# Kernel tuning notes

Hardware: AMD Instinct MI355X
Metric: run time of the kernel (lower is better)

The kernel has to match this reference:

```python
import jax, jax.numpy as jnp
import numpy as np

B, T, E, STRIDE = 32, 4096, 256, 16


def setup_inputs() -> dict:
    key = jax.random.key(0)
    nn_outs = jax.random.normal(key, (B, T, E), dtype=jnp.float32)
    # cut marker (==1) every STRIDE tokens, last position of each segment
    batch_x = jnp.zeros((B, T), dtype=jnp.int64).at[:, STRIDE - 1::STRIDE].set(1)
    return {"nn_outs": nn_outs, "batch_x": batch_x}


def reference(nn_outs, batch_x):
    """Hierarchical pooling: mean-pool nn_outs over segments delimited by
    batch_x == 1. Segment k of a row spans (cut_{k-1}, cut_k] inclusive of the
    cut token; tokens after the last cut are dropped (as in the original).
    Returns (pooled (B, maxlen, E), n_segments (B,))."""
    b, t, e = nn_outs.shape
    is_cut = (batch_x == 1)
    n_cuts = jnp.sum(is_cut, axis=1)                      # (B,) segments per row
    # exclusive cumsum: segment id of token t = #cuts strictly before t
    seg = jnp.cumsum(is_cut, axis=1) - is_cut.astype(jnp.int64)  # (B, T)
    valid = seg < n_cuts[:, None]                         # tokens after last cut dropped
    maxlen = int(jnp.max(n_cuts))                         # padded interm_step
    # flatten to global segment ids; invalid tokens go to a dump bucket
    gseg = jnp.where(valid, seg + jnp.arange(b, dtype=jnp.int64)[:, None] * maxlen,
                     b * maxlen)
    gseg = gseg.reshape(-1)
    flat = nn_outs.reshape(b * t, e)
    n_seg_total = b * maxlen + 1
    sums = jax.ops.segment_sum(flat, gseg, num_segments=n_seg_total)[:-1]
    counts = jax.ops.segment_sum(valid.reshape(-1).astype(nn_outs.dtype), gseg,
                                 num_segments=n_seg_total)[:-1]
    pooled = sums / jnp.maximum(counts, 1)[:, None]       # empty pad segments -> 0
    return pooled.reshape(b, maxlen, e), n_cuts
```

## Files before the change

### kernel.cpp

```cpp
#include <hip/hip_runtime.h>

#define NROWS 32
#define TLEN  4096
#define EDIM  256
#define PER   (TLEN / 256)
#define SEGS_PER_BLOCK 4

__global__ __launch_bounds__(256) void fused_pool_kernel(
    const float* __restrict__ nn,
    const int*  __restrict__ batch_x,
    int maxlen, int nb_per_row,
    float* __restrict__ out,
    float* __restrict__ n_cuts_out)
{
    const int tid  = threadIdx.x;
    const int lane = tid & 63;
    const int w    = tid >> 6;
    const int blk  = blockIdx.x;
    const int b    = blk / nb_per_row;
    const int k0   = (blk - b * nb_per_row) * SEGS_PER_BLOCK;

    __shared__ int s_cuts[TLEN];
    __shared__ int s_wsum[4];

    const int* row = batch_x + (long long)b * TLEN;
    const int t0 = tid * PER;

    int flags[PER];
#pragma unroll
    for (int j = 0; j < PER; j += 4) {
        const int4 v = *(const int4*)(row + t0 + j);
        flags[j] = v.x; flags[j + 1] = v.y; flags[j + 2] = v.z; flags[j + 3] = v.w;
    }
    int local = 0;
#pragma unroll
    for (int j = 0; j < PER; ++j) local += (flags[j] == 1);

    int incl = local;
#pragma unroll
    for (int d = 1; d < 64; d <<= 1) {
        const int v = __shfl_up(incl, d, 64);
        if (lane >= d) incl += v;
    }
    if (lane == 63) s_wsum[w] = incl;
    __syncthreads();
    const int s0 = s_wsum[0], s1 = s_wsum[1], s2 = s_wsum[2], s3 = s_wsum[3];
    const int wbase = (w > 0 ? s0 : 0) + (w > 1 ? s1 : 0) + (w > 2 ? s2 : 0);
    const int ncuts = s0 + s1 + s2 + s3;

    int idx = wbase + incl - local;
#pragma unroll
    for (int j = 0; j < PER; ++j)
        if (flags[j] == 1) s_cuts[idx++] = t0 + j;
    __syncthreads();

    if (k0 == 0 && tid == 0) n_cuts_out[b] = (float)ncuts;

    const int k = k0 + w;
    if (k >= maxlen) return;

    float4 acc = make_float4(0.f, 0.f, 0.f, 0.f);
    if (k < ncuts) {
        const int start = (k == 0) ? 0 : (s_cuts[k - 1] + 1);
        const int end   = s_cuts[k];
        const int cnt   = end - start + 1;
        const float* base = nn + ((long long)b * TLEN + start) * EDIM + lane * 4;

        if (cnt == 16) {
            float4 v[16];
#pragma unroll
            for (int t = 0; t < 16; ++t)
                v[t] = *(const float4*)(base + (long long)t * EDIM);
#pragma unroll
            for (int s = 1; s < 16; s <<= 1)
#pragma unroll
                for (int t = 0; t < 16; t += 2 * s) {
                    v[t].x += v[t + s].x; v[t].y += v[t + s].y;
                    v[t].z += v[t + s].z; v[t].w += v[t + s].w;
                }
            const float inv = 1.0f / 16.0f;
            acc.x = v[0].x * inv; acc.y = v[0].y * inv;
            acc.z = v[0].z * inv; acc.w = v[0].w * inv;
        } else {
            float4 a0 = make_float4(0.f, 0.f, 0.f, 0.f);
            float4 a1 = a0, a2 = a0, a3 = a0;
            int t = 0;
            for (; t + 4 <= cnt; t += 4) {
                const float4 v0 = *(const float4*)(base + (long long)(t + 0) * EDIM);
                const float4 v1 = *(const float4*)(base + (long long)(t + 1) * EDIM);
                const float4 v2 = *(const float4*)(base + (long long)(t + 2) * EDIM);
                const float4 v3 = *(const float4*)(base + (long long)(t + 3) * EDIM);
                a0.x += v0.x; a0.y += v0.y; a0.z += v0.z; a0.w += v0.w;
                a1.x += v1.x; a1.y += v1.y; a1.z += v1.z; a1.w += v1.w;
                a2.x += v2.x; a2.y += v2.y; a2.z += v2.z; a2.w += v2.w;
                a3.x += v3.x; a3.y += v3.y; a3.z += v3.z; a3.w += v3.w;
            }
            for (; t < cnt; ++t) {
                const float4 v = *(const float4*)(base + (long long)t * EDIM);
                a0.x += v.x; a0.y += v.y; a0.z += v.z; a0.w += v.w;
            }
            const float inv = 1.0f / (float)cnt;
            acc.x = ((a0.x + a1.x) + (a2.x + a3.x)) * inv;
            acc.y = ((a0.y + a1.y) + (a2.y + a3.y)) * inv;
            acc.z = ((a0.z + a1.z) + (a2.z + a3.z)) * inv;
            acc.w = ((a0.w + a1.w) + (a2.w + a3.w)) * inv;
        }
    }
    float4* o = (float4*)(out + ((long long)b * maxlen + k) * EDIM) + lane;
    *o = acc;
}

extern "C" void kernel_launch(void* const* d_in, const int* in_sizes, int n_in,
                              void* d_out, int out_size, void* d_ws, size_t ws_size,
                              hipStream_t stream) {
    const float* nn_outs = (const float*)d_in[0];
    const int*   batch_x = (const int*)d_in[1];
    float* out = (float*)d_out;

    const int B = NROWS;
    const int maxlen = (out_size - B) / (B * EDIM);
    float* n_cuts_out = out + (size_t)B * maxlen * EDIM;

    const int nb_per_row = (maxlen + SEGS_PER_BLOCK - 1) / SEGS_PER_BLOCK;
    const int blocks = B * nb_per_row;

    fused_pool_kernel<<<blocks, 256, 0, stream>>>(nn_outs, batch_x,
                                                  maxlen, nb_per_row,
                                                  out, n_cuts_out);
}
```

Before: 187.8 us.

## Speculatively prefetch segment data before cut scan, verify layout after

Each wave now issues its 16 row loads for segment k before the flag scan and barriers finish, guessing that segment k starts at token PER*k. This lets the global memory latency overlap with the prefix scan. If the guess is confirmed, those registers are reduced; otherwise the general path reloads from the real start. The flag handling also changes to a bitmask with popcount and ffs. The speculation only helps with evenly spaced cuts, and on mismatch it wastes bandwidth and uses more registers.

```diff
diff --git a/kernel.cpp b/kernel.cpp
--- a/kernel.cpp
+++ b/kernel.cpp
@@ -5,6 +5,8 @@
 #define EDIM  256
 #define PER   (TLEN / 256)
 #define SEGS_PER_BLOCK 4
+
+typedef float f32x4 __attribute__((ext_vector_type(4)));
 
 __global__ __launch_bounds__(256) void fused_pool_kernel(
     const float* __restrict__ nn,
@@ -19,6 +21,7 @@
     const int blk  = blockIdx.x;
     const int b    = blk / nb_per_row;
     const int k0   = (blk - b * nb_per_row) * SEGS_PER_BLOCK;
+    const int k    = k0 + w;
 
     __shared__ int s_cuts[TLEN];
     __shared__ int s_wsum[4];
@@ -26,21 +29,37 @@
     const int* row = batch_x + (long long)b * TLEN;
     const int t0 = tid * PER;
 
-    int flags[PER];
+    const int4 f0 = *(const int4*)(row + t0 + 0);
+    const int4 f1 = *(const int4*)(row + t0 + 4);
+    const int4 f2 = *(const int4*)(row + t0 + 8);
+    const int4 f3 = *(const int4*)(row + t0 + 12);
+
+    const int ps = PER * k;
+    const bool canpred = (k < maxlen) && (ps + PER <= TLEN);
+    f32x4 v[16];
+    if (canpred) {
+        const float* pbase = nn + ((long long)b * TLEN + ps) * EDIM + lane * 4;
 #pragma unroll
-    for (int j = 0; j < PER; j += 4) {
-        const int4 v = *(const int4*)(row + t0 + j);
-        flags[j] = v.x; flags[j + 1] = v.y; flags[j + 2] = v.z; flags[j + 3] = v.w;
+        for (int t = 0; t < 16; ++t)
+            v[t] = *(const f32x4*)(pbase + (long long)t * EDIM);
     }
-    int local = 0;
-#pragma unroll
-    for (int j = 0; j < PER; ++j) local += (flags[j] == 1);
+
+    unsigned mask = 0;
+    mask |= (unsigned)(f0.x == 1) << 0;  mask |= (unsigned)(f0.y == 1) << 1;
+    mask |= (unsigned)(f0.z == 1) << 2;  mask |= (unsigned)(f0.w == 1) << 3;
+    mask |= (unsigned)(f1.x == 1) << 4;  mask |= (unsigned)(f1.y == 1) << 5;
+    mask |= (unsigned)(f1.z == 1) << 6;  mask |= (unsigned)(f1.w == 1) << 7;
+    mask |= (unsigned)(f2.x == 1) << 8;  mask |= (unsigned)(f2.y == 1) << 9;
+    mask |= (unsigned)(f2.z == 1) << 10; mask |= (unsigned)(f2.w == 1) << 11;
+    mask |= (unsigned)(f3.x == 1) << 12; mask |= (unsigned)(f3.y == 1) << 13;
+    mask |= (unsigned)(f3.z == 1) << 14; mask |= (unsigned)(f3.w == 1) << 15;
+    const int local = __popc(mask);
 
     int incl = local;
 #pragma unroll
     for (int d = 1; d < 64; d <<= 1) {
-        const int v = __shfl_up(incl, d, 64);
-        if (lane >= d) incl += v;
+        const int vv = __shfl_up(incl, d, 64);
+        if (lane >= d) incl += vv;
     }
     if (lane == 63) s_wsum[w] = incl;
     __syncthreads();
@@ -49,65 +68,48 @@
     const int ncuts = s0 + s1 + s2 + s3;
 
     int idx = wbase + incl - local;
-#pragma unroll
-    for (int j = 0; j < PER; ++j)
-        if (flags[j] == 1) s_cuts[idx++] = t0 + j;
+    unsigned m = mask;
+    while (m) {
+        const int j = __ffs(m) - 1;
+        m &= m - 1;
+        s_cuts[idx++] = t0 + j;
+    }
     __syncthreads();
 
     if (k0 == 0 && tid == 0) n_cuts_out[b] = (float)ncuts;
 
-    const int k = k0 + w;
     if (k >= maxlen) return;
 
-    float4 acc = make_float4(0.f, 0.f, 0.f, 0.f);
+    f32x4 acc = {0.f, 0.f, 0.f, 0.f};
     if (k < ncuts) {
         const int start = (k == 0) ? 0 : (s_cuts[k - 1] + 1);
         const int end   = s_cuts[k];
         const int cnt   = end - start + 1;
-        const float* base = nn + ((long long)b * TLEN + start) * EDIM + lane * 4;
 
-        if (cnt == 16) {
-            float4 v[16];
-#pragma unroll
-            for (int t = 0; t < 16; ++t)
-                v[t] = *(const float4*)(base + (long long)t * EDIM);
+        if (canpred && start == ps && cnt == PER) {
 #pragma unroll
             for (int s = 1; s < 16; s <<= 1)
 #pragma unroll
-                for (int t = 0; t < 16; t += 2 * s) {
-                    v[t].x += v[t + s].x; v[t].y += v[t + s].y;
-                    v[t].z += v[t + s].z; v[t].w += v[t + s].w;
-                }
-            const float inv = 1.0f / 16.0f;
-            acc.x = v[0].x * inv; acc.y = v[0].y * inv;
-            acc.z = v[0].z * inv; acc.w = v[0].w * inv;
+                for (int t = 0; t < 16; t += 2 * s)
+                    v[t] += v[t + s];
+            acc = v[0] * (1.0f / (float)PER);
         } else {
-            float4 a0 = make_float4(0.f, 0.f, 0.f, 0.f);
-            float4 a1 = a0, a2 = a0, a3 = a0;
+            const float* base = nn + ((long long)b * TLEN + start) * EDIM + lane * 4;
+            f32x4 a0 = {0.f, 0.f, 0.f, 0.f};
+            f32x4 a1 = a0, a2 = a0, a3 = a0;
             int t = 0;
             for (; t + 4 <= cnt; t += 4) {
-                const float4 v0 = *(const float4*)(base + (long long)(t + 0) * EDIM);
-                const float4 v1 = *(const float4*)(base + (long long)(t + 1) * EDIM);
-                const float4 v2 = *(const float4*)(base + (long long)(t + 2) * EDIM);
-                const float4 v3 = *(const float4*)(base + (long long)(t + 3) * EDIM);
-                a0.x += v0.x; a0.y += v0.y; a0.z += v0.z; a0.w += v0.w;
-                a1.x += v1.x; a1.y += v1.y; a1.z += v1.z; a1.w += v1.w;
-                a2.x += v2.x; a2.y += v2.y; a2.z += v2.z; a2.w += v2.w;
-                a3.x += v3.x; a3.y += v3.y; a3.z += v3.z; a3.w += v3.w;
+                a0 += *(const f32x4*)(base + (long long)(t + 0) * EDIM);
+                a1 += *(const f32x4*)(base + (long long)(t + 1) * EDIM);
+                a2 += *(const f32x4*)(base + (long long)(t + 2) * EDIM);
+                a3 += *(const f32x4*)(base + (long long)(t + 3) * EDIM);
             }
-            for (; t < cnt; ++t) {
-                const float4 v = *(const float4*)(base + (long long)t * EDIM);
-                a0.x += v.x; a0.y += v.y; a0.z += v.z; a0.w += v.w;
-            }
-            const float inv = 1.0f / (float)cnt;
-            acc.x = ((a0.x + a1.x) + (a2.x + a3.x)) * inv;
-            acc.y = ((a0.y + a1.y) + (a2.y + a3.y)) * inv;
-            acc.z = ((a0.z + a1.z) + (a2.z + a3.z)) * inv;
-            acc.w = ((a0.w + a1.w) + (a2.w + a3.w)) * inv;
+            for (; t < cnt; ++t)
+                a0 += *(const f32x4*)(base + (long long)t * EDIM);
+            acc = ((a0 + a1) + (a2 + a3)) * (1.0f / (float)cnt);
         }
     }
-    float4* o = (float4*)(out + ((long long)b * maxlen + k) * EDIM) + lane;
-    *o = acc;
+    *((f32x4*)(out + ((long long)b * maxlen + k) * EDIM) + lane) = acc;
 }
 
 extern "C" void kernel_launch(void* const* d_in, const int* in_sizes, int n_in,
```

Result: slower. 191.9 us (+2.2%).
